# Kernel tuning notes

Measured on AMD Instinct MI355X. Metric: run time of the kernel, lower is better.

The kernel has to match this reference:

```python
import math
import jax, jax.numpy as jnp
import numpy as np

B, T, DIM, H = 2, 2048, 2048, 16
D = DIM // H  # head_dim = 128


def setup_inputs() -> dict:
    key = jax.random.key(0)
    ks = jax.random.split(key, 6)
    s = 0.02
    x = jax.random.normal(ks[0], (B, T, DIM), dtype=jnp.float32)
    # causal mask: True = keep, False = masked (matches masked_fill(mask==0, -inf))
    attn_mask = jnp.tril(jnp.ones((T, T), dtype=bool))[None, None, :, :]
    Wq = jax.random.normal(ks[1], (DIM, DIM), dtype=jnp.float32) * s
    Wk = jax.random.normal(ks[2], (DIM, D), dtype=jnp.float32) * s
    Wv = jax.random.normal(ks[3], (DIM, D), dtype=jnp.float32) * s
    Wo = jax.random.normal(ks[4], (DIM, DIM), dtype=jnp.float32) * s
    return {
        "x": x, "attn_mask": attn_mask,
        "Wq": Wq, "bq": jnp.zeros((DIM,), jnp.float32),
        "Wk": Wk, "bk": jnp.zeros((D,), jnp.float32),
        "Wv": Wv, "bv": jnp.zeros((D,), jnp.float32),
        "Wo": Wo, "bo": jnp.zeros((DIM,), jnp.float32),
    }


def _rope_freqs(t_len, d):
    inv_freq = 1.0 / (10000.0 ** (jnp.arange(0, d, 2, dtype=jnp.float32) / d))
    f = jnp.arange(t_len, dtype=jnp.float32)[:, None] * inv_freq[None, :]  # [T, d/2]
    # duplicate to full head dim so cos/sin align with rotate_half's half split
    cos = jnp.concatenate([jnp.cos(f), jnp.cos(f)], axis=-1)[None, None]  # [1,1,T,d]
    sin = jnp.concatenate([jnp.sin(f), jnp.sin(f)], axis=-1)[None, None]
    return cos, sin


def _rotate_half(u):
    d2 = u.shape[-1] // 2
    return jnp.concatenate([-u[..., d2:], u[..., :d2]], axis=-1)


def reference(x, attn_mask, Wq, bq, Wk, bk, Wv, bv, Wo, bo):
    Bx, Tx, C = x.shape
    q = (x @ Wq + bq).reshape(Bx, Tx, H, D).transpose(0, 2, 1, 3)  # [B,H,T,D]
    k = (x @ Wk + bk)[:, None]  # [B,1,T,D] single shared KV head (MQA)
    v = (x @ Wv + bv)[:, None]
    cos, sin = _rope_freqs(Tx, D)
    q = q * cos + _rotate_half(q) * sin
    k = k * cos + _rotate_half(k) * sin
    attn = jnp.matmul(q, k.swapaxes(-2, -1)) / math.sqrt(D)  # [B,H,T,T]
    attn = jnp.where(attn_mask, attn, jnp.float32(-jnp.inf))
    attn = jax.nn.softmax(attn, axis=-1)
    out = jnp.matmul(attn, v)  # [B,H,T,D]
    out = out.transpose(0, 2, 1, 3).reshape(Bx, Tx, C)
    return out @ Wo + bo
```

## Files before the change

kernel.cpp:

```cpp
#include <hip/hip_runtime.h>

typedef unsigned short u16;
typedef unsigned int u32;
typedef __bf16 bf16x8 __attribute__((ext_vector_type(8)));
typedef float f32x4 __attribute__((ext_vector_type(4)));
typedef float f32x16 __attribute__((ext_vector_type(16)));
typedef u32 u32x4 __attribute__((ext_vector_type(4)));

__device__ __forceinline__ u16 bfu(float x) {
  union { __bf16 h; u16 u; } z; z.h = (__bf16)x; return z.u;
}
__device__ __forceinline__ u32 pk2(float a, float b) {
  union { __bf16 h[2]; u32 u; } z;
  z.h[0] = (__bf16)a; z.h[1] = (__bf16)b;
  return z.u;
}
__device__ __forceinline__ void gl_lds16(const u16* g, u16* l) {
  __builtin_amdgcn_global_load_lds((const __attribute__((address_space(1))) void*)g,
                                   (__attribute__((address_space(3))) void*)l, 16, 0, 0);
}

__global__ __launch_bounds__(256) void cvt_bf16(const float* __restrict__ src, u16* __restrict__ dst, int n8) {
  int i = blockIdx.x * 256 + threadIdx.x;
  if (i >= n8) return;
  const float4* s4 = (const float4*)src;
  float4 a = s4[2 * i], b = s4[2 * i + 1];
  u32x4 o;
  o[0] = pk2(a.x, a.y); o[1] = pk2(a.z, a.w);
  o[2] = pk2(b.x, b.y); o[3] = pk2(b.z, b.w);
  ((u32x4*)dst)[i] = o;
}

__global__ void transpose_cvt(const float* __restrict__ src, u16* __restrict__ dst, int R, int C) {
  __shared__ float tile[32][33];
  const int c0 = blockIdx.x * 32, r0 = blockIdx.y * 32;
  const int tx = threadIdx.x, ty = threadIdx.y;
#pragma unroll
  for (int i = 0; i < 4; ++i)
    tile[ty + i * 8][tx] = src[(size_t)(r0 + ty + i * 8) * C + c0 + tx];
  __syncthreads();
#pragma unroll
  for (int i = 0; i < 4; ++i)
    dst[(size_t)(c0 + ty + i * 8) * R + r0 + tx] = bfu(tile[tx][ty + i * 8]);
}

__global__ void transpose_v16(const u16* __restrict__ Vrow, u16* __restrict__ Vt) {
  __shared__ u16 tile[32][33];
  const int t0 = blockIdx.x * 32, d0 = blockIdx.y * 32, b = blockIdx.z;
  const int tx = threadIdx.x, ty = threadIdx.y;
#pragma unroll
  for (int i = 0; i < 4; ++i)
    tile[ty + i * 8][tx] = Vrow[(size_t)(b * 2048 + t0 + ty + i * 8) * 128 + d0 + tx];
  __syncthreads();
#pragma unroll
  for (int i = 0; i < 4; ++i)
    Vt[(size_t)b * 262144 + (size_t)(d0 + ty + i * 8) * 2048 + t0 + tx] = tile[tx][ty + i * 8];
}

__global__ __launch_bounds__(256) void gemm_qkv(const u16* __restrict__ A, const u16* __restrict__ Bt,
                                                const float* __restrict__ bq, const float* __restrict__ bk,
                                                const float* __restrict__ bv,
                                                u16* __restrict__ Qb, u16* __restrict__ Kb,
                                                u16* __restrict__ Vrow) {
  const int lin = blockIdx.x;
  const int xcd = lin & 7, idx = lin >> 3;
  const int ly = idx / 9, lx = idx - ly * 9;
  const int my = (xcd >> 1) * 8 + ly;
  const int nt = (xcd & 1) * 9 + lx;
  const int n0 = nt * 128, m0 = my * 128;
  const int K = 2048;
  const int tid = threadIdx.x, lane = tid & 63;
  const int wid = tid >> 6;
  __shared__ __align__(16) u16 As[128 * 32];
  __shared__ __align__(16) u16 Bs[128 * 32];
  f32x4 acc[2][8];
#pragma unroll
  for (int i = 0; i < 2; ++i)
#pragma unroll
    for (int j = 0; j < 8; ++j)
#pragma unroll
      for (int rr = 0; rr < 4; ++rr) acc[i][j][rr] = 0.f;

  const int c0 = tid, c1 = tid + 256;
  const int ar0 = c0 >> 2, ac0 = (c0 & 3) * 8;
  const int ar1 = c1 >> 2, ac1 = (c1 & 3) * 8;
  const int r = lane & 15, g = lane >> 4;

  for (int k0 = 0; k0 < K; k0 += 32) {
    gl_lds16(A + (size_t)(m0 + ar0) * K + k0 + ac0, As + c0 * 8);
    gl_lds16(A + (size_t)(m0 + ar1) * K + k0 + ac1, As + c1 * 8);
    gl_lds16(Bt + (size_t)(n0 + ar0) * K + k0 + ac0, Bs + c0 * 8);
    gl_lds16(Bt + (size_t)(n0 + ar1) * K + k0 + ac1, Bs + c1 * 8);
    __syncthreads();
    bf16x8 af[2], bfr[8];
#pragma unroll
    for (int mi = 0; mi < 2; ++mi)
      af[mi] = *reinterpret_cast<const bf16x8*>(&As[(wid * 32 + mi * 16 + r) * 32 + g * 8]);
#pragma unroll
    for (int ni = 0; ni < 8; ++ni)
      bfr[ni] = *reinterpret_cast<const bf16x8*>(&Bs[(ni * 16 + r) * 32 + g * 8]);
#pragma unroll
    for (int mi = 0; mi < 2; ++mi)
#pragma unroll
      for (int ni = 0; ni < 8; ++ni)
        acc[mi][ni] = __builtin_amdgcn_mfma_f32_16x16x32_bf16(af[mi], bfr[ni], acc[mi][ni], 0, 0, 0);
    __syncthreads();
  }

  const float nl2 = -0.20762050593046f;
  if (nt < 17) {
    const bool isQ = (nt < 16);
    const float sc = isQ ? 0.1275173862437171f : 1.0f;
    const float* bias = isQ ? (bq + nt * 128) : bk;
    u16* dst = isQ ? Qb : Kb;
#pragma unroll
    for (int mi = 0; mi < 2; ++mi)
#pragma unroll
      for (int reg = 0; reg < 4; ++reg) {
        const int row = m0 + wid * 32 + mi * 16 + g * 4 + reg;
        const int b = row >> 11, t = row & 2047;
#pragma unroll
        for (int ni = 0; ni < 4; ++ni) {
          const int j = ni * 16 + r;
          const float v0 = acc[mi][ni][reg] + bias[j];
          const float v1 = acc[mi][ni + 4][reg] + bias[j + 64];
          const float ang = (float)t * exp2f((float)j * nl2);
          float s, c;
          __sincosf(ang, &s, &c);
          const size_t base = isQ ? (((size_t)((b * 16 + nt) * 2048 + t)) * 128 + j)
                                  : (((size_t)(b * 2048 + t)) * 128 + j);
          dst[base]      = bfu((v0 * c - v1 * s) * sc);
          dst[base + 64] = bfu((v1 * c + v0 * s) * sc);
        }
      }
  } else {
#pragma unroll
    for (int mi = 0; mi < 2; ++mi)
#pragma unroll
      for (int reg = 0; reg < 4; ++reg) {
        const int row = m0 + wid * 32 + mi * 16 + g * 4 + reg;
#pragma unroll
        for (int ni = 0; ni < 8; ++ni) {
          const int d = ni * 16 + r;
          Vrow[(size_t)row * 128 + d] = bfu(acc[mi][ni][reg] + bv[d]);
        }
      }
  }
}

template <bool BIAS>
__global__ __launch_bounds__(256) void gemm_bt(const u16* __restrict__ A, const u16* __restrict__ Bt,
                                               const float* __restrict__ bias, float* __restrict__ C,
                                               int M, int N, int K) {
  const int lin = blockIdx.x;
  const int xcd = lin & 7, idx = lin >> 3;
  const int my = (xcd >> 1) * 8 + (idx >> 3);
  const int nx = (xcd & 1) * 8 + (idx & 7);
  const int n0 = nx * 128, m0 = my * 128;
  const int tid = threadIdx.x, lane = tid & 63;
  const int wid = tid >> 6, wr = wid >> 1, wc = wid & 1;
  __shared__ __align__(16) u16 As[128 * 32];
  __shared__ __align__(16) u16 Bs[128 * 32];
  f32x4 acc[4][4];
#pragma unroll
  for (int i = 0; i < 4; ++i)
#pragma unroll
    for (int j = 0; j < 4; ++j)
#pragma unroll
      for (int rr = 0; rr < 4; ++rr) acc[i][j][rr] = 0.f;

  const int c0 = tid, c1 = tid + 256;
  const int ar0 = c0 >> 2, ac0 = (c0 & 3) * 8;
  const int ar1 = c1 >> 2, ac1 = (c1 & 3) * 8;
  const int r = lane & 15, g = lane >> 4;

  for (int k0 = 0; k0 < K; k0 += 32) {
    gl_lds16(A + (size_t)(m0 + ar0) * K + k0 + ac0, As + c0 * 8);
    gl_lds16(A + (size_t)(m0 + ar1) * K + k0 + ac1, As + c1 * 8);
    gl_lds16(Bt + (size_t)(n0 + ar0) * K + k0 + ac0, Bs + c0 * 8);
    gl_lds16(Bt + (size_t)(n0 + ar1) * K + k0 + ac1, Bs + c1 * 8);
    __syncthreads();
    bf16x8 af[4], bfr[4];
#pragma unroll
    for (int mi = 0; mi < 4; ++mi)
      af[mi] = *reinterpret_cast<const bf16x8*>(&As[(wr * 64 + mi * 16 + r) * 32 + g * 8]);
#pragma unroll
    for (int ni = 0; ni < 4; ++ni)
      bfr[ni] = *reinterpret_cast<const bf16x8*>(&Bs[(wc * 64 + ni * 16 + r) * 32 + g * 8]);
#pragma unroll
    for (int mi = 0; mi < 4; ++mi)
#pragma unroll
      for (int ni = 0; ni < 4; ++ni)
        acc[mi][ni] = __builtin_amdgcn_mfma_f32_16x16x32_bf16(af[mi], bfr[ni], acc[mi][ni], 0, 0, 0);
    __syncthreads();
  }
#pragma unroll
  for (int mi = 0; mi < 4; ++mi)
#pragma unroll
    for (int ni = 0; ni < 4; ++ni) {
      int col = n0 + wc * 64 + ni * 16 + r;
      float bia = BIAS ? bias[col] : 0.f;
#pragma unroll
      for (int reg = 0; reg < 4; ++reg) {
        int row = m0 + wr * 64 + mi * 16 + g * 4 + reg;
        C[(size_t)row * N + col] = acc[mi][ni][reg] + bia;
      }
    }
}

__global__ __launch_bounds__(256, 2) void attn_kernel(const u16* __restrict__ Qb, const u16* __restrict__ Kb,
                                                      const u16* __restrict__ Vt, u16* __restrict__ Ob) {
  const int bid = blockIdx.x;
  const int grp = bid >> 5;
  const int chunk = (bid < 256) ? (15 - grp) : (grp - 8);
  const int bh = bid & 31, h = bh & 15, b = bh >> 4;
  const int tid = threadIdx.x, wid = tid >> 6, lane = tid & 63;
  const int l31 = lane & 31, hf = lane >> 5;

  __shared__ __align__(16) u16 smem[32768];
  u16* Ksb = smem;
  u16* Vsb = smem + 16384;

  const u16* Kbase = Kb + (size_t)b * 2048 * 128;
  const u16* Vbase = Vt + (size_t)b * 128 * 2048;

  int krow[4], kcol[4], vrow[4], vcol[4];
#pragma unroll
  for (int i = 0; i < 4; ++i) {
    const int seg = wid * 4 + i;
    const int r = seg * 4 + (lane >> 4);
    krow[i] = r; kcol[i] = (((lane & 15) ^ (r & 15)) << 3);
    const int d = seg * 8 + (lane >> 3);
    vrow[i] = d; vcol[i] = (((lane & 7) ^ (d & 7)) << 3);
  }
  const int ldsoff = wid * 2048 + lane * 8;

#define STAGE(buf, kvb_) do {                                                              \
    _Pragma("unroll") for (int i_ = 0; i_ < 4; ++i_)                                       \
      gl_lds16(Kbase + (size_t)((kvb_) + krow[i_]) * 128 + kcol[i_],                       \
               &Ksb[(buf) * 8192 + ldsoff + i_ * 512]);                                    \
    _Pragma("unroll") for (int i_ = 0; i_ < 4; ++i_)                                       \
      gl_lds16(Vbase + (size_t)vrow[i_] * 2048 + (kvb_) + vcol[i_],                        \
               &Vsb[(buf) * 8192 + ldsoff + i_ * 512]);                                    \
  } while (0)

  const int xk16 = l31 & 15;
  const int xk8 = l31 & 7;

  const int cb = chunk * 128;
  const int qw = cb + wid * 32;
  const u16* qptr = Qb + ((size_t)((b * 16 + h) * 2048 + qw + l31)) * 128;
  bf16x8 qf[8];
#pragma unroll
  for (int c = 0; c < 8; ++c)
    qf[c] = *reinterpret_cast<const bf16x8*>(qptr + c * 16 + hf * 8);

  f32x16 ot[4];
#pragma unroll
  for (int dt = 0; dt < 4; ++dt)
#pragma unroll
    for (int rr = 0; rr < 16; ++rr) ot[dt][rr] = 0.f;
  float m = -1e30f, lsum = 0.f;

  const int nkv = 2 * chunk + 2;
  STAGE(0, 0);
  for (int it = 0; it < nkv; ++it) {
    const int kvb = it << 6, cur = it & 1;
    if (it + 1 < nkv) {
      STAGE(cur ^ 1, kvb + 64);
      asm volatile("s_waitcnt vmcnt(8)" ::: "memory");
    } else {
      asm volatile("s_waitcnt vmcnt(0)" ::: "memory");
    }
    __builtin_amdgcn_s_barrier();

    if (kvb <= qw) {
      const u16* ks = Ksb + cur * 8192;
      const u16* vs = Vsb + cur * 8192;
      f32x16 st0, st1;
#pragma unroll
      for (int rr = 0; rr < 16; ++rr) { st0[rr] = 0.f; st1[rr] = -1e30f; }
      const u16* ksr0 = ks + l31 * 128;
#pragma unroll
      for (int c = 0; c < 8; ++c) {
        bf16x8 kf = *reinterpret_cast<const bf16x8*>(ksr0 + (((2 * c + hf) ^ xk16) << 3));
        st0 = __builtin_amdgcn_mfma_f32_32x32x16_bf16(kf, qf[c], st0, 0, 0, 0);
      }
      const bool a1 = (kvb + 32 <= qw);
      if (a1) {
#pragma unroll
        for (int rr = 0; rr < 16; ++rr) st1[rr] = 0.f;
        const u16* ksr1 = ks + (32 + l31) * 128;
#pragma unroll
        for (int c = 0; c < 8; ++c) {
          bf16x8 kf = *reinterpret_cast<const bf16x8*>(ksr1 + (((2 * c + hf) ^ xk16) << 3));
          st1 = __builtin_amdgcn_mfma_f32_32x32x16_bf16(kf, qf[c], st1, 0, 0, 0);
        }
        if (kvb + 32 == qw) {
#pragma unroll
          for (int rr = 0; rr < 16; ++rr) {
            int kvl = (rr & 3) + 8 * (rr >> 2) + 4 * hf;
            if (kvl > l31) st1[rr] = -1e30f;
          }
        }
      }
      if (kvb == qw) {
#pragma unroll
        for (int rr = 0; rr < 16; ++rr) {
          int kvl = (rr & 3) + 8 * (rr >> 2) + 4 * hf;
          if (kvl > l31) st0[rr] = -1e30f;
        }
      }

      float tmax = st0[0];
#pragma unroll
      for (int rr = 1; rr < 16; ++rr) tmax = fmaxf(tmax, st0[rr]);
#pragma unroll
      for (int rr = 0; rr < 16; ++rr) tmax = fmaxf(tmax, st1[rr]);
      tmax = fmaxf(tmax, __shfl_xor(tmax, 32, 64));
      if (!__all(tmax - m <= 8.f)) {
        const float mnew = fmaxf(m, tmax);
        const float alpha = exp2f(m - mnew);
        lsum *= alpha;
#pragma unroll
        for (int dt = 0; dt < 4; ++dt)
#pragma unroll
          for (int rr = 0; rr < 16; ++rr) ot[dt][rr] *= alpha;
        m = mnew;
      }
      float rsum = 0.f;
#pragma unroll
      for (int rr = 0; rr < 16; ++rr) { st0[rr] = exp2f(st0[rr] - m); rsum += st0[rr]; }
#pragma unroll
      for (int rr = 0; rr < 16; ++rr) { st1[rr] = exp2f(st1[rr] - m); rsum += st1[rr]; }
      rsum += __shfl_xor(rsum, 32, 64);
      lsum += rsum;

#pragma unroll
      for (int n = 0; n < 2; ++n) {
        if (n == 1 && !a1) break;
        const f32x16& pp = n ? st1 : st0;
#pragma unroll
        for (int s = 0; s < 2; ++s) {
          u32 a0p = pk2(pp[8 * s + 0], pp[8 * s + 1]);
          u32 a1p = pk2(pp[8 * s + 2], pp[8 * s + 3]);
          u32 b0p = pk2(pp[8 * s + 4], pp[8 * s + 5]);
          u32 b1p = pk2(pp[8 * s + 6], pp[8 * s + 7]);
          u32 k0 = hf ? b0p : a0p, k1 = hf ? b1p : a1p;
          u32 sd0 = hf ? a0p : b0p, sd1 = hf ? a1p : b1p;
          u32 r0 = (u32)__shfl_xor((int)sd0, 32, 64);
          u32 r1 = (u32)__shfl_xor((int)sd1, 32, 64);
          u32x4 pw;
          pw[0] = hf ? r0 : k0; pw[1] = hf ? r1 : k1;
          pw[2] = hf ? k0 : r0; pw[3] = hf ? k1 : r1;
          bf16x8 pb = __builtin_bit_cast(bf16x8, pw);
          const int cc = n * 4 + s * 2 + hf;
#pragma unroll
          for (int dt = 0; dt < 4; ++dt) {
            bf16x8 vf = *reinterpret_cast<const bf16x8*>(
                &vs[(dt * 32 + l31) * 64 + ((cc ^ xk8) << 3)]);
            ot[dt] = __builtin_amdgcn_mfma_f32_32x32x16_bf16(vf, pb, ot[dt], 0, 0, 0);
          }
        }
      }
    }
    __builtin_amdgcn_s_barrier();
  }

  u16* myt = smem + wid * (32 * 136);
  const float inv = 1.f / lsum;
#pragma unroll
  for (int dt = 0; dt < 4; ++dt)
#pragma unroll
    for (int rq = 0; rq < 4; ++rq) {
      int d = dt * 32 + 8 * rq + 4 * hf;
      u32 lo = pk2(ot[dt][rq * 4 + 0] * inv, ot[dt][rq * 4 + 1] * inv);
      u32 hi = pk2(ot[dt][rq * 4 + 2] * inv, ot[dt][rq * 4 + 3] * inv);
      u32* dstp = (u32*)&myt[l31 * 136 + d];
      dstp[0] = lo; dstp[1] = hi;
    }
  __syncthreads();
  const size_t outbase = ((size_t)(b * 2048 + qw)) * 2048 + h * 128;
#pragma unroll
  for (int i = 0; i < 8; ++i) {
    int chunk2 = i * 64 + lane;
    int row = chunk2 >> 4, c16 = chunk2 & 15;
    u32x4 v = *reinterpret_cast<const u32x4*>(&myt[row * 136 + c16 * 8]);
    *reinterpret_cast<u32x4*>(Ob + outbase + (size_t)row * 2048 + c16 * 8) = v;
  }
#undef STAGE
}

extern "C" void kernel_launch(void* const* d_in, const int* in_sizes, int n_in,
                              void* d_out, int out_size, void* d_ws, size_t ws_size,
                              hipStream_t stream) {
  const float* x  = (const float*)d_in[0];
  const float* Wq = (const float*)d_in[2];
  const float* bq = (const float*)d_in[3];
  const float* Wk = (const float*)d_in[4];
  const float* bk = (const float*)d_in[5];
  const float* Wv = (const float*)d_in[6];
  const float* bv = (const float*)d_in[7];
  const float* Wo = (const float*)d_in[8];
  const float* bo = (const float*)d_in[9];

  char* ws = (char*)d_ws;
  u16*  xb    = (u16*)ws;   ws += (size_t)4096 * 2048 * 2;
  u16*  WqkvT = (u16*)ws;   ws += (size_t)2304 * 2048 * 2;
  u16*  WoT   = (u16*)ws;   ws += (size_t)2048 * 2048 * 2;
  u16*  Qb    = (u16*)ws;   ws += (size_t)2 * 16 * 2048 * 128 * 2;
  u16*  Kb    = (u16*)ws;   ws += (size_t)2 * 2048 * 128 * 2;
  u16*  Vrow  = (u16*)ws;   ws += (size_t)2 * 2048 * 128 * 2;
  u16*  Vt    = (u16*)ws;   ws += (size_t)2 * 128 * 2048 * 2;
  u16*  Ob    = (u16*)ws;   ws += (size_t)4096 * 2048 * 2;

  dim3 tb(32, 8);
  cvt_bf16<<<4096, 256, 0, stream>>>(x, xb, 1048576);
  transpose_cvt<<<dim3(64, 64), tb, 0, stream>>>(Wq, WqkvT, 2048, 2048);
  transpose_cvt<<<dim3(4, 64),  tb, 0, stream>>>(Wk, WqkvT + (size_t)2048 * 2048, 2048, 128);
  transpose_cvt<<<dim3(4, 64),  tb, 0, stream>>>(Wv, WqkvT + (size_t)2176 * 2048, 2048, 128);
  transpose_cvt<<<dim3(64, 64), tb, 0, stream>>>(Wo, WoT, 2048, 2048);

  gemm_qkv<<<576, 256, 0, stream>>>(xb, WqkvT, bq, bk, bv, Qb, Kb, Vrow);
  transpose_v16<<<dim3(64, 4, 2), tb, 0, stream>>>(Vrow, Vt);
  attn_kernel<<<512, 256, 0, stream>>>(Qb, Kb, Vt, Ob);
  gemm_bt<true><<<512, 256, 0, stream>>>(Ob, WoT, bo, (float*)d_out, 4096, 2048, 2048);
}
```

Before: 237.0 us.

## Double-buffer LDS tiles in QKV and output GEMMs to overlap loads

Both GEMM kernels now use two LDS buffers for A and B. Each iteration issues the global-to-LDS load for the next K-slice before computing on the current one, then waits with a partial vmcnt so the four newest loads can stay in flight. This hides global memory latency behind MFMA work and doubles the LDS footprint. The synchronisation relies on hand-written s_waitcnt plus raw s_barrier instead of __syncthreads, which is fragile if the compiler reorders LDS reads around those points.

```diff
diff --git a/kernel.cpp b/kernel.cpp
--- a/kernel.cpp
+++ b/kernel.cpp
@@ -71,8 +71,8 @@
   const int K = 2048;
   const int tid = threadIdx.x, lane = tid & 63;
   const int wid = tid >> 6;
-  __shared__ __align__(16) u16 As[128 * 32];
-  __shared__ __align__(16) u16 Bs[128 * 32];
+  __shared__ __align__(16) u16 As[2 * 128 * 32];
+  __shared__ __align__(16) u16 Bs[2 * 128 * 32];
   f32x4 acc[2][8];
 #pragma unroll
   for (int i = 0; i < 2; ++i)
@@ -86,26 +86,41 @@
   const int ar1 = c1 >> 2, ac1 = (c1 & 3) * 8;
   const int r = lane & 15, g = lane >> 4;
 
-  for (int k0 = 0; k0 < K; k0 += 32) {
-    gl_lds16(A + (size_t)(m0 + ar0) * K + k0 + ac0, As + c0 * 8);
-    gl_lds16(A + (size_t)(m0 + ar1) * K + k0 + ac1, As + c1 * 8);
-    gl_lds16(Bt + (size_t)(n0 + ar0) * K + k0 + ac0, Bs + c0 * 8);
-    gl_lds16(Bt + (size_t)(n0 + ar1) * K + k0 + ac1, Bs + c1 * 8);
-    __syncthreads();
+#define QSTAGE(buf, k0_) do {                                                   \
+    gl_lds16(A + (size_t)(m0 + ar0) * K + (k0_) + ac0, As + (buf) * 4096 + c0 * 8); \
+    gl_lds16(A + (size_t)(m0 + ar1) * K + (k0_) + ac1, As + (buf) * 4096 + c1 * 8); \
+    gl_lds16(Bt + (size_t)(n0 + ar0) * K + (k0_) + ac0, Bs + (buf) * 4096 + c0 * 8); \
+    gl_lds16(Bt + (size_t)(n0 + ar1) * K + (k0_) + ac1, Bs + (buf) * 4096 + c1 * 8); \
+  } while (0)
+
+  const int NT = K / 32;
+  QSTAGE(0, 0);
+  for (int t = 0; t < NT; ++t) {
+    const int cur = t & 1;
+    if (t + 1 < NT) {
+      QSTAGE(cur ^ 1, (t + 1) * 32);
+      asm volatile("s_waitcnt vmcnt(4)" ::: "memory");
+    } else {
+      asm volatile("s_waitcnt vmcnt(0)" ::: "memory");
+    }
+    __builtin_amdgcn_s_barrier();
+    const u16* as = As + cur * 4096;
+    const u16* bs = Bs + cur * 4096;
     bf16x8 af[2], bfr[8];
 #pragma unroll
     for (int mi = 0; mi < 2; ++mi)
-      af[mi] = *reinterpret_cast<const bf16x8*>(&As[(wid * 32 + mi * 16 + r) * 32 + g * 8]);
+      af[mi] = *reinterpret_cast<const bf16x8*>(&as[(wid * 32 + mi * 16 + r) * 32 + g * 8]);
 #pragma unroll
     for (int ni = 0; ni < 8; ++ni)
-      bfr[ni] = *reinterpret_cast<const bf16x8*>(&Bs[(ni * 16 + r) * 32 + g * 8]);
+      bfr[ni] = *reinterpret_cast<const bf16x8*>(&bs[(ni * 16 + r) * 32 + g * 8]);
 #pragma unroll
     for (int mi = 0; mi < 2; ++mi)
 #pragma unroll
       for (int ni = 0; ni < 8; ++ni)
         acc[mi][ni] = __builtin_amdgcn_mfma_f32_16x16x32_bf16(af[mi], bfr[ni], acc[mi][ni], 0, 0, 0);
-    __syncthreads();
-  }
+    __builtin_amdgcn_s_barrier();
+  }
+#undef QSTAGE
 
   const float nl2 = -0.20762050593046f;
   if (nt < 17) {
@@ -159,8 +174,8 @@
   const int n0 = nx * 128, m0 = my * 128;
   const int tid = threadIdx.x, lane = tid & 63;
   const int wid = tid >> 6, wr = wid >> 1, wc = wid & 1;
-  __shared__ __align__(16) u16 As[128 * 32];
-  __shared__ __align__(16) u16 Bs[128 * 32];
+  __shared__ __align__(16) u16 As[2 * 128 * 32];
+  __shared__ __align__(16) u16 Bs[2 * 128 * 32];
   f32x4 acc[4][4];
 #pragma unroll
   for (int i = 0; i < 4; ++i)
@@ -174,26 +189,42 @@
   const int ar1 = c1 >> 2, ac1 = (c1 & 3) * 8;
   const int r = lane & 15, g = lane >> 4;
 
-  for (int k0 = 0; k0 < K; k0 += 32) {
-    gl_lds16(A + (size_t)(m0 + ar0) * K + k0 + ac0, As + c0 * 8);
-    gl_lds16(A + (size_t)(m0 + ar1) * K + k0 + ac1, As + c1 * 8);
-    gl_lds16(Bt + (size_t)(n0 + ar0) * K + k0 + ac0, Bs + c0 * 8);
-    gl_lds16(Bt + (size_t)(n0 + ar1) * K + k0 + ac1, Bs + c1 * 8);
-    __syncthreads();
+#define OSTAGE(buf, k0_) do {                                                   \
+    gl_lds16(A + (size_t)(m0 + ar0) * K + (k0_) + ac0, As + (buf) * 4096 + c0 * 8); \
+    gl_lds16(A + (size_t)(m0 + ar1) * K + (k0_) + ac1, As + (buf) * 4096 + c1 * 8); \
+    gl_lds16(Bt + (size_t)(n0 + ar0) * K + (k0_) + ac0, Bs + (buf) * 4096 + c0 * 8); \
+    gl_lds16(Bt + (size_t)(n0 + ar1) * K + (k0_) + ac1, Bs + (buf) * 4096 + c1 * 8); \
+  } while (0)
+
+  const int NT = K / 32;
+  OSTAGE(0, 0);
+  for (int t = 0; t < NT; ++t) {
+    const int cur = t & 1;
+    if (t + 1 < NT) {
+      OSTAGE(cur ^ 1, (t + 1) * 32);
+      asm volatile("s_waitcnt vmcnt(4)" ::: "memory");
+    } else {
+      asm volatile("s_waitcnt vmcnt(0)" ::: "memory");
+    }
+    __builtin_amdgcn_s_barrier();
+    const u16* as = As + cur * 4096;
+    const u16* bs = Bs + cur * 4096;
     bf16x8 af[4], bfr[4];
 #pragma unroll
     for (int mi = 0; mi < 4; ++mi)
-      af[mi] = *reinterpret_cast<const bf16x8*>(&As[(wr * 64 + mi * 16 + r) * 32 + g * 8]);
+      af[mi] = *reinterpret_cast<const bf16x8*>(&as[(wr * 64 + mi * 16 + r) * 32 + g * 8]);
 #pragma unroll
     for (int ni = 0; ni < 4; ++ni)
-      bfr[ni] = *reinterpret_cast<const bf16x8*>(&Bs[(wc * 64 + ni * 16 + r) * 32 + g * 8]);
+      bfr[ni] = *reinterpret_cast<const bf16x8*>(&bs[(wc * 64 + ni * 16 + r) * 32 + g * 8]);
 #pragma unroll
     for (int mi = 0; mi < 4; ++mi)
 #pragma unroll
       for (int ni = 0; ni < 4; ++ni)
         acc[mi][ni] = __builtin_amdgcn_mfma_f32_16x16x32_bf16(af[mi], bfr[ni], acc[mi][ni], 0, 0, 0);
-    __syncthreads();
-  }
+    __builtin_amdgcn_s_barrier();
+  }
+#undef OSTAGE
+
 #pragma unroll
   for (int mi = 0; mi < 4; ++mi)
 #pragma unroll
```

Measured after the change: 248.3 us. +4.8%, slower.
